# Performance work log

Measured on AMD Instinct MI355X. Metric: run time of the kernel, lower is better.

## Reference

```python
import jax, jax.numpy as jnp
import numpy as np

B, T, D, H = 2, 2048, 1024, 16
DH = D // H

def setup_inputs() -> dict:
    key = jax.random.key(0)
    ks = jax.random.split(key, 5)
    scale = 1.0 / np.sqrt(D)
    x = jax.random.normal(ks[0], (B, T, D), dtype=jnp.float32)
    Wq = jax.random.normal(ks[1], (D, D), dtype=jnp.float32) * scale
    Wk = jax.random.normal(ks[2], (D, D), dtype=jnp.float32) * scale
    Wv = jax.random.normal(ks[3], (D, D), dtype=jnp.float32) * scale
    Wo = jax.random.normal(ks[4], (D, D), dtype=jnp.float32) * scale
    # causal mask: True means masked (matches torch masked_fill semantics)
    mask = jnp.triu(jnp.ones((T, T), dtype=bool), k=1)
    return {"x": x, "mask": mask, "Wq": Wq, "Wk": Wk, "Wv": Wv, "Wo": Wo}

def reference(x, mask, Wq, Wk, Wv, Wo):
    b, t, c = x.shape
    # projections -> [B, H, T, DH]
    def split_heads(y):
        return y.reshape(b, t, H, DH).transpose(0, 2, 1, 3)
    q = split_heads(x @ Wq)
    k = split_heads(x @ Wk)
    v = split_heads(x @ Wv)
    # scores [B, H, T, T]
    att = jnp.einsum('bhqd,bhkd->bhqk', q, k) / jnp.sqrt(jnp.float32(DH))
    att = jnp.where(mask, -jnp.inf, att)
    att = jax.nn.softmax(att, axis=-1)
    # dropout=0.0 (eval-mode determinism)
    out = jnp.einsum('bhqk,bhkd->bhqd', att, v)
    out = out.transpose(0, 2, 1, 3).reshape(b, t, c)
    return out @ Wo
```

## Files before the change

kernel.cpp:

```cpp
#include <hip/hip_runtime.h>
#include <stdint.h>

typedef unsigned short u16;
typedef unsigned int u32;
typedef __attribute__((ext_vector_type(8))) short s16x8;
typedef __attribute__((ext_vector_type(4))) float f32x4;
typedef __attribute__((ext_vector_type(8))) unsigned short u16x8;
typedef __attribute__((ext_vector_type(4))) unsigned short u16x4;

#define T_ 2048
#define D_ 1024
#define H_ 16
#define DH_ 64

#define QSCALE_LOG2E 0.18033688011112042f

#if __has_builtin(__builtin_amdgcn_exp2f)
#define EXP2(x) __builtin_amdgcn_exp2f(x)
#else
#define EXP2(x) exp2f(x)
#endif

__device__ __forceinline__ float bf2f(u16 u) {
    union { unsigned int i; float f; } x; x.i = ((unsigned int)u) << 16; return x.f;
}
__device__ __forceinline__ u16 f2bf(float f) {
    union { float f; unsigned int i; } x; x.f = f;
    unsigned int u = x.i;
    u += 0x7fffu + ((u >> 16) & 1u);
    return (u16)(u >> 16);
}
__device__ __forceinline__ u32 pack_rn(float a, float b) {
    union { float f; u32 u; } ua, ub; ua.f = a; ub.f = b;
    return ((ua.u + 0x8000u) >> 16) | ((ub.u + 0x8000u) & 0xffff0000u);
}

__device__ __forceinline__ void gload16(const u16* g, u16* l) {
    __builtin_amdgcn_global_load_lds(
        (const __attribute__((address_space(1))) void*)g,
        (__attribute__((address_space(3))) void*)l,
        16, 0, 0);
}

__global__ __launch_bounds__(256) void cvt_x_kernel(const float* __restrict__ x,
                                                    u16* __restrict__ xb) {
    int i = (blockIdx.x * 256 + threadIdx.x) * 4;
    float4 v = *(const float4*)(x + i);
    u16x4 o;
    o[0] = f2bf(v.x); o[1] = f2bf(v.y); o[2] = f2bf(v.z); o[3] = f2bf(v.w);
    *(u16x4*)(xb + i) = o;
}

__global__ __launch_bounds__(256) void transpose_w_kernel(const float* __restrict__ Wq,
                                                          const float* __restrict__ Wk,
                                                          const float* __restrict__ Wv,
                                                          const float* __restrict__ Wo,
                                                          u16* __restrict__ WT) {
    __shared__ float tile[32][33];
    int s = blockIdx.z;
    const float* W = (s == 0) ? Wq : (s == 1) ? Wk : (s == 2) ? Wv : Wo;
    int n0 = blockIdx.x * 32;
    int k0 = blockIdx.y * 32;
    int tx = threadIdx.x, ty = threadIdx.y;
    #pragma unroll
    for (int j = 0; j < 32; j += 8)
        tile[ty + j][tx] = W[(k0 + ty + j) * D_ + n0 + tx];
    __syncthreads();
    u16* dst = WT + (size_t)s * D_ * D_;
    #pragma unroll
    for (int j = 0; j < 32; j += 8)
        dst[(n0 + ty + j) * D_ + k0 + tx] = f2bf(tile[tx][ty + j]);
}

__global__ __launch_bounds__(256) void gemm_qkv(const u16* __restrict__ A,
                                                const u16* __restrict__ Bt,
                                                u16* __restrict__ Qw,
                                                u16* __restrict__ Kw,
                                                u16* __restrict__ Vw) {
    __shared__ __align__(16) u16 As[2][128 * 32];
    __shared__ __align__(16) u16 Bs[2][128 * 32];
    const int m0 = blockIdx.x * 128, n0 = blockIdx.y * 128;
    int tid = threadIdx.x;
    int w = tid >> 6, lane = tid & 63, quad = lane >> 4, l15 = lane & 15;
    int wr = w >> 1, wc = w & 1;

    int nb0 = (w << 7), nb1 = nb0 + 64;
    int c0 = nb0 + lane, c1 = nb1 + lane;
    int r0 = c0 >> 2, k0off = (c0 & 3) << 3;
    int r1 = c1 >> 2, k1off = (c1 & 3) << 3;
    const u16* Ar0 = A + (size_t)(m0 + r0) * D_ + k0off;
    const u16* Ar1 = A + (size_t)(m0 + r1) * D_ + k1off;
    const u16* Br0 = Bt + (size_t)(n0 + r0) * D_ + k0off;
    const u16* Br1 = Bt + (size_t)(n0 + r1) * D_ + k1off;

    f32x4 acc[4][4];
    #pragma unroll
    for (int mi = 0; mi < 4; ++mi)
        #pragma unroll
        for (int ni = 0; ni < 4; ++ni) acc[mi][ni] = (f32x4){0.f, 0.f, 0.f, 0.f};

    gload16(Ar0, &As[0][nb0 << 3]);
    gload16(Ar1, &As[0][nb1 << 3]);
    gload16(Br0, &Bs[0][nb0 << 3]);
    gload16(Br1, &Bs[0][nb1 << 3]);

    for (int k0 = 0; k0 < D_; k0 += 32) {
        int buf = (k0 >> 5) & 1;
        __syncthreads();
        if (k0 + 32 < D_) {
            int kn = k0 + 32;
            gload16(Ar0 + kn, &As[buf ^ 1][nb0 << 3]);
            gload16(Ar1 + kn, &As[buf ^ 1][nb1 << 3]);
            gload16(Br0 + kn, &Bs[buf ^ 1][nb0 << 3]);
            gload16(Br1 + kn, &Bs[buf ^ 1][nb1 << 3]);
        }
        s16x8 af[4], bf[4];
        #pragma unroll
        for (int mi = 0; mi < 4; ++mi)
            af[mi] = *(const s16x8*)&As[buf][((wr * 64 + mi * 16 + l15) << 5) + (quad << 3)];
        #pragma unroll
        for (int ni = 0; ni < 4; ++ni)
            bf[ni] = *(const s16x8*)&Bs[buf][((wc * 64 + ni * 16 + l15) << 5) + (quad << 3)];
        #pragma unroll
        for (int mi = 0; mi < 4; ++mi)
            #pragma unroll
            for (int ni = 0; ni < 4; ++ni)
                acc[mi][ni] = __builtin_amdgcn_mfma_f32_16x16x32_bf16(af[mi], bf[ni],
                                                                      acc[mi][ni], 0, 0, 0);
    }

    #pragma unroll
    for (int mi = 0; mi < 4; ++mi) {
        int mbase = m0 + wr * 64 + mi * 16 + quad * 4;
        #pragma unroll
        for (int ni = 0; ni < 4; ++ni) {
            int n = n0 + wc * 64 + ni * 16 + l15;
            int b = mbase >> 11, t0 = mbase & 2047;
            int sel = n >> 10, nn = n & 1023;
            int h = nn >> 6, dh = nn & 63;
            int bhidx = (b << 4) + h;
            if (sel == 0) {
                #pragma unroll
                for (int r = 0; r < 4; ++r)
                    Qw[(size_t)(bhidx * T_ + t0 + r) * DH_ + dh] =
                        f2bf(acc[mi][ni][r] * QSCALE_LOG2E);
            } else if (sel == 1) {
                #pragma unroll
                for (int r = 0; r < 4; ++r)
                    Kw[(size_t)(bhidx * T_ + t0 + r) * DH_ + dh] = f2bf(acc[mi][ni][r]);
            } else {
                uint2 pk;
                pk.x = pack_rn(acc[mi][ni][0], acc[mi][ni][1]);
                pk.y = pack_rn(acc[mi][ni][2], acc[mi][ni][3]);
                *(uint2*)(Vw + ((size_t)bhidx * DH_ + dh) * T_ + t0) = pk;
            }
        }
    }
}

__global__ __launch_bounds__(256) void gemm_out(const u16* __restrict__ A,
                                                const u16* __restrict__ Bt,
                                                float* __restrict__ Cout) {
    __shared__ __align__(16) u16 As[2][128 * 32];
    __shared__ __align__(16) u16 Bs[2][64 * 32];
    const int m0 = blockIdx.x * 128, n0 = blockIdx.y * 64;
    int tid = threadIdx.x;
    int w = tid >> 6, lane = tid & 63, quad = lane >> 4, l15 = lane & 15;

    int nbA0 = (w << 7), nbA1 = nbA0 + 64, nbB = (w << 6);
    int cA0 = nbA0 + lane, cA1 = nbA1 + lane, cB = nbB + lane;
    const u16* ArA0 = A + (size_t)(m0 + (cA0 >> 2)) * D_ + ((cA0 & 3) << 3);
    const u16* ArA1 = A + (size_t)(m0 + (cA1 >> 2)) * D_ + ((cA1 & 3) << 3);
    const u16* BrB  = Bt + (size_t)(n0 + (cB >> 2)) * D_ + ((cB & 3) << 3);

    f32x4 acc[2][4];
    #pragma unroll
    for (int mi = 0; mi < 2; ++mi)
        #pragma unroll
        for (int ni = 0; ni < 4; ++ni) acc[mi][ni] = (f32x4){0.f, 0.f, 0.f, 0.f};

    gload16(ArA0, &As[0][nbA0 << 3]);
    gload16(ArA1, &As[0][nbA1 << 3]);
    gload16(BrB,  &Bs[0][nbB << 3]);

    for (int k0 = 0; k0 < D_; k0 += 32) {
        int buf = (k0 >> 5) & 1;
        __syncthreads();
        if (k0 + 32 < D_) {
            int kn = k0 + 32;
            gload16(ArA0 + kn, &As[buf ^ 1][nbA0 << 3]);
            gload16(ArA1 + kn, &As[buf ^ 1][nbA1 << 3]);
            gload16(BrB + kn,  &Bs[buf ^ 1][nbB << 3]);
        }
        s16x8 af[2], bf[4];
        #pragma unroll
        for (int mi = 0; mi < 2; ++mi)
            af[mi] = *(const s16x8*)&As[buf][((w * 32 + mi * 16 + l15) << 5) + (quad << 3)];
        #pragma unroll
        for (int ni = 0; ni < 4; ++ni)
            bf[ni] = *(const s16x8*)&Bs[buf][((ni * 16 + l15) << 5) + (quad << 3)];
        #pragma unroll
        for (int mi = 0; mi < 2; ++mi)
            #pragma unroll
            for (int ni = 0; ni < 4; ++ni)
                acc[mi][ni] = __builtin_amdgcn_mfma_f32_16x16x32_bf16(af[mi], bf[ni],
                                                                      acc[mi][ni], 0, 0, 0);
    }

    #pragma unroll
    for (int mi = 0; mi < 2; ++mi) {
        int mbase = m0 + w * 32 + mi * 16 + quad * 4;
        #pragma unroll
        for (int ni = 0; ni < 4; ++ni) {
            int n = n0 + ni * 16 + l15;
            #pragma unroll
            for (int r = 0; r < 4; ++r)
                Cout[(size_t)(mbase + r) * D_ + n] = acc[mi][ni][r];
        }
    }
}

__global__ __launch_bounds__(256) void attn_mfma_kernel(const u16* __restrict__ Qg,
                                                        const u16* __restrict__ Kg,
                                                        const u16* __restrict__ Vt,
                                                        u16* __restrict__ Opart,
                                                        float* __restrict__ lpart) {
    __shared__ __align__(16) u16 Kbuf[2][64 * 64];
    __shared__ __align__(16) u16 Vbuf[2][64 * 64];
    __shared__ __align__(16) u16 Ps[4][2][16][72];

    int blk = blockIdx.x;
    int xcd = blk & 7, slot = blk >> 3;
    int bh = (xcd << 2) + (slot / 40);
    int x  = slot % 40;
    int BX, c;
    if (x < 4)       { BX = x;                    c = 0; }
    else if (x < 12) { BX = 4 + ((x - 4) >> 1);   c = (x - 4) & 1; }
    else if (x < 24) { BX = 8 + (x - 12) / 3;     c = (x - 12) % 3; }
    else             { BX = 12 + ((x - 24) >> 2); c = (x - 24) & 3; }
    int kstart = c << 3;
    int ktm = 2 * BX + 1;
    int kend = min(kstart + 8, ktm + 1);

    int tid = threadIdx.x;
    int w = tid >> 6, lane = tid & 63, quad = lane >> 4, l15 = lane & 15;
    int q0 = BX << 7;
    int qA = q0 + 16 * w;
    int qB = q0 + 64 + 16 * w;

    const u16* Qb = Qg + (size_t)bh * T_ * DH_;
    const u16* Kb = Kg + (size_t)bh * T_ * DH_;
    const u16* Vb = Vt + (size_t)bh * DH_ * T_;

    s16x8 qa0 = *(const s16x8*)(Qb + (size_t)(qA + l15) * DH_ + quad * 8);
    s16x8 qa1 = *(const s16x8*)(Qb + (size_t)(qA + l15) * DH_ + quad * 8 + 32);
    s16x8 qc0 = *(const s16x8*)(Qb + (size_t)(qB + l15) * DH_ + quad * 8);
    s16x8 qc1 = *(const s16x8*)(Qb + (size_t)(qB + l15) * DH_ + quad * 8 + 32);

    int nb0 = (w << 7), nb1 = nb0 + 64;
    int n0c = nb0 + lane, n1c = nb1 + lane;
    int r0 = n0c >> 3, c0s = n0c & 7, g0 = (r0 << 3) + (c0s ^ (r0 & 7));
    int r1 = n1c >> 3, c1s = n1c & 7, g1 = (r1 << 3) + (c1s ^ (r1 & 7));

    {
        int kb0 = kstart << 6;
        const u16* Ktile = Kb + (size_t)kb0 * DH_;
        gload16(Ktile + (g0 << 3), &Kbuf[0][nb0 << 3]);
        gload16(Ktile + (g1 << 3), &Kbuf[0][nb1 << 3]);
        gload16(Vb + (size_t)r0 * T_ + kb0 + ((g0 & 7) << 3), &Vbuf[0][nb0 << 3]);
        gload16(Vb + (size_t)r1 * T_ + kb0 + ((g1 & 7) << 3), &Vbuf[0][nb1 << 3]);
    }

    f32x4 oA[4] = {{0.f,0.f,0.f,0.f},{0.f,0.f,0.f,0.f},{0.f,0.f,0.f,0.f},{0.f,0.f,0.f,0.f}};
    f32x4 oB[4] = {{0.f,0.f,0.f,0.f},{0.f,0.f,0.f,0.f},{0.f,0.f,0.f,0.f},{0.f,0.f,0.f,0.f}};
    float lA = 0.f, lB = 0.f;

    for (int kt = kstart; kt < kend; ++kt) {
        int buf = (kt - kstart) & 1;
        __syncthreads();

        if (kt + 1 < kend) {
            int kb2 = (kt + 1) << 6;
            const u16* Ktile = Kb + (size_t)kb2 * DH_;
            gload16(Ktile + (g0 << 3), &Kbuf[buf ^ 1][nb0 << 3]);
            gload16(Ktile + (g1 << 3), &Kbuf[buf ^ 1][nb1 << 3]);
            gload16(Vb + (size_t)r0 * T_ + kb2 + ((g0 & 7) << 3), &Vbuf[buf ^ 1][nb0 << 3]);
            gload16(Vb + (size_t)r1 * T_ + kb2 + ((g1 & 7) << 3), &Vbuf[buf ^ 1][nb1 << 3]);
        }

        f32x4 sA[4], sB[4];
        #pragma unroll
        for (int g = 0; g < 4; ++g) {
            int r = (g << 4) + l15;
            int cc = quad ^ (r & 7);
            s16x8 ka0 = *(const s16x8*)&Kbuf[buf][((r << 3) + cc) << 3];
            s16x8 ka1 = *(const s16x8*)&Kbuf[buf][((r << 3) + (cc ^ 4)) << 3];
            f32x4 z = {0.f, 0.f, 0.f, 0.f};
            sA[g] = __builtin_amdgcn_mfma_f32_16x16x32_bf16(ka0, qa0, z, 0, 0, 0);
            sA[g] = __builtin_amdgcn_mfma_f32_16x16x32_bf16(ka1, qa1, sA[g], 0, 0, 0);
            sB[g] = __builtin_amdgcn_mfma_f32_16x16x32_bf16(ka0, qc0, z, 0, 0, 0);
            sB[g] = __builtin_amdgcn_mfma_f32_16x16x32_bf16(ka1, qc1, sB[g], 0, 0, 0);
        }

        if (kt >= ktm - 1) {
            int rA = q0 + 16 * w + l15 - (kt << 6);
            #pragma unroll
            for (int g = 0; g < 4; ++g)
                #pragma unroll
                for (int r = 0; r < 4; ++r)
                    if ((g << 4) + (quad << 2) + r > rA) sA[g][r] = -INFINITY;
        }
        if (kt == ktm) {
            int rB = 16 * w + l15;
            #pragma unroll
            for (int g = 0; g < 4; ++g)
                #pragma unroll
                for (int r = 0; r < 4; ++r)
                    if ((g << 4) + (quad << 2) + r > rB) sB[g][r] = -INFINITY;
        }

        #pragma unroll
        for (int g = 0; g < 4; ++g)
            #pragma unroll
            for (int r = 0; r < 4; ++r) {
                float pA = EXP2(sA[g][r]); sA[g][r] = pA; lA += pA;
                float pB = EXP2(sB[g][r]); sB[g][r] = pB; lB += pB;
            }

        #pragma unroll
        for (int g = 0; g < 4; ++g) {
            uint2 pkA, pkB;
            pkA.x = pack_rn(sA[g][0], sA[g][1]); pkA.y = pack_rn(sA[g][2], sA[g][3]);
            pkB.x = pack_rn(sB[g][0], sB[g][1]); pkB.y = pack_rn(sB[g][2], sB[g][3]);
            *(uint2*)&Ps[w][0][l15][g * 16 + quad * 4] = pkA;
            *(uint2*)&Ps[w][1][l15][g * 16 + quad * 4] = pkB;
        }
        s16x8 pa0 = *(const s16x8*)&Ps[w][0][l15][quad * 8];
        s16x8 pa1 = *(const s16x8*)&Ps[w][0][l15][quad * 8 + 32];
        s16x8 pc0 = *(const s16x8*)&Ps[w][1][l15][quad * 8];
        s16x8 pc1 = *(const s16x8*)&Ps[w][1][l15][quad * 8 + 32];

        #pragma unroll
        for (int g = 0; g < 4; ++g) {
            int r = (g << 4) + l15;
            int cc = quad ^ (r & 7);
            s16x8 va0 = *(const s16x8*)&Vbuf[buf][((r << 3) + cc) << 3];
            s16x8 va1 = *(const s16x8*)&Vbuf[buf][((r << 3) + (cc ^ 4)) << 3];
            oA[g] = __builtin_amdgcn_mfma_f32_16x16x32_bf16(va0, pa0, oA[g], 0, 0, 0);
            oA[g] = __builtin_amdgcn_mfma_f32_16x16x32_bf16(va1, pa1, oA[g], 0, 0, 0);
            oB[g] = __builtin_amdgcn_mfma_f32_16x16x32_bf16(va0, pc0, oB[g], 0, 0, 0);
            oB[g] = __builtin_amdgcn_mfma_f32_16x16x32_bf16(va1, pc1, oB[g], 0, 0, 0);
        }
    }

    lA += __shfl_xor(lA, 16); lA += __shfl_xor(lA, 32);
    lB += __shfl_xor(lB, 16); lB += __shfl_xor(lB, 32);
    int slotid = ((bh << 4) + BX) * 4 + c;
    u16* dA = Opart + ((size_t)slotid * 128 + 16 * w + l15) * 64;
    u16* dB = dA + 64 * 64;
    #pragma unroll
    for (int g = 0; g < 4; ++g) {
        uint2 pk;
        pk.x = pack_rn(oA[g][0], oA[g][1]); pk.y = pack_rn(oA[g][2], oA[g][3]);
        *(uint2*)(dA + (g << 4) + (quad << 2)) = pk;
        pk.x = pack_rn(oB[g][0], oB[g][1]); pk.y = pack_rn(oB[g][2], oB[g][3]);
        *(uint2*)(dB + (g << 4) + (quad << 2)) = pk;
    }
    if (quad == 0) {
        lpart[(size_t)slotid * 128 + 16 * w + l15] = lA;
        lpart[(size_t)slotid * 128 + 64 + 16 * w + l15] = lB;
    }
}

__global__ __launch_bounds__(256) void reduce_attn(const u16* __restrict__ Opart,
                                                   const float* __restrict__ lpart,
                                                   u16* __restrict__ att) {
    int BX = blockIdx.x, bh = blockIdx.y;
    int nch = (BX >> 2) + 1;
    int tid = threadIdx.x;
    int row = tid >> 1, dh0 = (tid & 1) << 5;
    int slotbase = ((bh << 4) + BX) << 2;

    float acc[32];
    #pragma unroll
    for (int i = 0; i < 32; ++i) acc[i] = 0.f;
    float l = 0.f;
    for (int cc = 0; cc < nch; ++cc) {
        const u16* op = Opart + ((size_t)(slotbase + cc) * 128 + row) * 64 + dh0;
        #pragma unroll
        for (int v = 0; v < 4; ++v) {
            u16x8 o8 = *(const u16x8*)(op + v * 8);
            #pragma unroll
            for (int j = 0; j < 8; ++j) acc[v * 8 + j] += bf2f(o8[j]);
        }
        l += lpart[(size_t)(slotbase + cc) * 128 + row];
    }
    float inv = 1.f / l;
    int b = bh >> 4, h = bh & 15;
    int q = (BX << 7) + row;
    u16* dst = att + ((size_t)(b * T_) + q) * D_ + (h << 6) + dh0;
    #pragma unroll
    for (int v = 0; v < 2; ++v) {
        u16x8 o8;
        #pragma unroll
        for (int j = 0; j < 8; ++j) o8[j] = f2bf(acc[v * 16 + j * 2] * inv),
                                    o8[j] = o8[j];
        #pragma unroll
        for (int j = 0; j < 8; ++j) o8[j] = f2bf(acc[v * 16 + j] * inv);
        u16x8 o8b;
        #pragma unroll
        for (int j = 0; j < 8; ++j) o8b[j] = f2bf(acc[v * 16 + 8 + j] * inv);
        *(u16x8*)(dst + v * 16) = o8;
        *(u16x8*)(dst + v * 16 + 8) = o8b;
    }
}

extern "C" void kernel_launch(void* const* d_in, const int* in_sizes, int n_in,
                              void* d_out, int out_size, void* d_ws, size_t ws_size,
                              hipStream_t stream) {
    const float* x  = (const float*)d_in[0];
    const float* Wq = (const float*)d_in[2];
    const float* Wk = (const float*)d_in[3];
    const float* Wv = (const float*)d_in[4];
    const float* Wo = (const float*)d_in[5];
    float* out = (float*)d_out;

    char* ws = (char*)d_ws;
    u16*   xb    = (u16*)(ws);
    u16*   WT    = (u16*)(ws + (8ull  << 20));
    u16*   Qw    = (u16*)(ws + (16ull << 20));
    u16*   Kw    = (u16*)(ws + (24ull << 20));
    u16*   Vw    = (u16*)(ws + (32ull << 20));
    u16*   att   = (u16*)(ws + (40ull << 20));
    u16*   Opart = (u16*)(ws + (48ull << 20));
    float* lpart = (float*)(ws + (82ull << 20));

    cvt_x_kernel<<<dim3(4096), dim3(256), 0, stream>>>(x, xb);
    transpose_w_kernel<<<dim3(32, 32, 4), dim3(32, 8), 0, stream>>>(Wq, Wk, Wv, Wo, WT);
    gemm_qkv<<<dim3(32, 24), dim3(256), 0, stream>>>(xb, WT, Qw, Kw, Vw);
    attn_mfma_kernel<<<dim3(1280), dim3(256), 0, stream>>>(Qw, Kw, Vw, Opart, lpart);
    reduce_attn<<<dim3(16, 32), dim3(256), 0, stream>>>(Opart, lpart, att);
    gemm_out<<<dim3(32, 16), dim3(256), 0, stream>>>(att, WT + 3ull * 1048576ull, out);
}
```

Measured before the change: 200.0 us.

## Swizzle GEMM LDS tiles and merge input preparation kernels

Applies an XOR swizzle to the k-chunk placement in the LDS tiles of both projection GEMMs, so that fragment reads no longer hit the same banks. The swizzle is applied on the global source offset, so the direct-to-LDS loads stay linear. The x conversion and the weight transpose are merged into one launch, and the reduce store loop is simplified. This adds index arithmetic per load.

Measured after the change: 195.2 us. -2.4%, faster.

```diff
diff --git a/kernel.cpp b/kernel.cpp
--- a/kernel.cpp
+++ b/kernel.cpp
@@ -42,34 +42,37 @@
         16, 0, 0);
 }
 
-__global__ __launch_bounds__(256) void cvt_x_kernel(const float* __restrict__ x,
-                                                    u16* __restrict__ xb) {
-    int i = (blockIdx.x * 256 + threadIdx.x) * 4;
-    float4 v = *(const float4*)(x + i);
-    u16x4 o;
-    o[0] = f2bf(v.x); o[1] = f2bf(v.y); o[2] = f2bf(v.z); o[3] = f2bf(v.w);
-    *(u16x4*)(xb + i) = o;
-}
-
-__global__ __launch_bounds__(256) void transpose_w_kernel(const float* __restrict__ Wq,
-                                                          const float* __restrict__ Wk,
-                                                          const float* __restrict__ Wv,
-                                                          const float* __restrict__ Wo,
-                                                          u16* __restrict__ WT) {
+__global__ __launch_bounds__(256) void prep_kernel(const float* __restrict__ x,
+                                                   const float* __restrict__ Wq,
+                                                   const float* __restrict__ Wk,
+                                                   const float* __restrict__ Wv,
+                                                   const float* __restrict__ Wo,
+                                                   u16* __restrict__ xb,
+                                                   u16* __restrict__ WT) {
     __shared__ float tile[32][33];
-    int s = blockIdx.z;
-    const float* W = (s == 0) ? Wq : (s == 1) ? Wk : (s == 2) ? Wv : Wo;
-    int n0 = blockIdx.x * 32;
-    int k0 = blockIdx.y * 32;
-    int tx = threadIdx.x, ty = threadIdx.y;
-    #pragma unroll
-    for (int j = 0; j < 32; j += 8)
-        tile[ty + j][tx] = W[(k0 + ty + j) * D_ + n0 + tx];
-    __syncthreads();
-    u16* dst = WT + (size_t)s * D_ * D_;
-    #pragma unroll
-    for (int j = 0; j < 32; j += 8)
-        dst[(n0 + ty + j) * D_ + k0 + tx] = f2bf(tile[tx][ty + j]);
+    int blk = blockIdx.x;
+    if (blk < 4096) {
+        int i = (blk * 256 + threadIdx.x) * 4;
+        float4 v = *(const float4*)(x + i);
+        u16x4 o;
+        o[0] = f2bf(v.x); o[1] = f2bf(v.y); o[2] = f2bf(v.z); o[3] = f2bf(v.w);
+        *(u16x4*)(xb + i) = o;
+    } else {
+        int t = blk - 4096;
+        int s = t >> 10;
+        const float* W = (s == 0) ? Wq : (s == 1) ? Wk : (s == 2) ? Wv : Wo;
+        int n0 = ((t >> 5) & 31) * 32;
+        int k0 = (t & 31) * 32;
+        int tx = threadIdx.x & 31, ty = threadIdx.x >> 5;
+        #pragma unroll
+        for (int j = 0; j < 32; j += 8)
+            tile[ty + j][tx] = W[(k0 + ty + j) * D_ + n0 + tx];
+        __syncthreads();
+        u16* dst = WT + (size_t)s * D_ * D_;
+        #pragma unroll
+        for (int j = 0; j < 32; j += 8)
+            dst[(n0 + ty + j) * D_ + k0 + tx] = f2bf(tile[tx][ty + j]);
+    }
 }
 
 __global__ __launch_bounds__(256) void gemm_qkv(const u16* __restrict__ A,
@@ -86,8 +89,8 @@
 
     int nb0 = (w << 7), nb1 = nb0 + 64;
     int c0 = nb0 + lane, c1 = nb1 + lane;
-    int r0 = c0 >> 2, k0off = (c0 & 3) << 3;
-    int r1 = c1 >> 2, k1off = (c1 & 3) << 3;
+    int r0 = c0 >> 2, k0off = (((c0 & 3) ^ ((r0 >> 1) & 3)) << 3);
+    int r1 = c1 >> 2, k1off = (((c1 & 3) ^ ((r1 >> 1) & 3)) << 3);
     const u16* Ar0 = A + (size_t)(m0 + r0) * D_ + k0off;
     const u16* Ar1 = A + (size_t)(m0 + r1) * D_ + k1off;
     const u16* Br0 = Bt + (size_t)(n0 + r0) * D_ + k0off;
@@ -116,11 +119,15 @@
         }
         s16x8 af[4], bf[4];
         #pragma unroll
-        for (int mi = 0; mi < 4; ++mi)
-            af[mi] = *(const s16x8*)&As[buf][((wr * 64 + mi * 16 + l15) << 5) + (quad << 3)];
-        #pragma unroll
-        for (int ni = 0; ni < 4; ++ni)
-            bf[ni] = *(const s16x8*)&Bs[buf][((wc * 64 + ni * 16 + l15) << 5) + (quad << 3)];
+        for (int mi = 0; mi < 4; ++mi) {
+            int R = wr * 64 + mi * 16 + l15;
+            af[mi] = *(const s16x8*)&As[buf][((R << 2) | (quad ^ ((R >> 1) & 3))) << 3];
+        }
+        #pragma unroll
+        for (int ni = 0; ni < 4; ++ni) {
+            int R = wc * 64 + ni * 16 + l15;
+            bf[ni] = *(const s16x8*)&Bs[buf][((R << 2) | (quad ^ ((R >> 1) & 3))) << 3];
+        }
         #pragma unroll
         for (int mi = 0; mi < 4; ++mi)
             #pragma unroll
@@ -169,9 +176,12 @@
 
     int nbA0 = (w << 7), nbA1 = nbA0 + 64, nbB = (w << 6);
     int cA0 = nbA0 + lane, cA1 = nbA1 + lane, cB = nbB + lane;
-    const u16* ArA0 = A + (size_t)(m0 + (cA0 >> 2)) * D_ + ((cA0 & 3) << 3);
-    const u16* ArA1 = A + (size_t)(m0 + (cA1 >> 2)) * D_ + ((cA1 & 3) << 3);
-    const u16* BrB  = Bt + (size_t)(n0 + (cB >> 2)) * D_ + ((cB & 3) << 3);
+    int rA0 = cA0 >> 2, kA0 = (((cA0 & 3) ^ ((rA0 >> 1) & 3)) << 3);
+    int rA1 = cA1 >> 2, kA1 = (((cA1 & 3) ^ ((rA1 >> 1) & 3)) << 3);
+    int rB  = cB >> 2,  kB  = (((cB  & 3) ^ ((rB  >> 1) & 3)) << 3);
+    const u16* ArA0 = A + (size_t)(m0 + rA0) * D_ + kA0;
+    const u16* ArA1 = A + (size_t)(m0 + rA1) * D_ + kA1;
+    const u16* BrB  = Bt + (size_t)(n0 + rB) * D_ + kB;
 
     f32x4 acc[2][4];
     #pragma unroll
@@ -194,11 +204,15 @@
         }
         s16x8 af[2], bf[4];
         #pragma unroll
-        for (int mi = 0; mi < 2; ++mi)
-            af[mi] = *(const s16x8*)&As[buf][((w * 32 + mi * 16 + l15) << 5) + (quad << 3)];
-        #pragma unroll
-        for (int ni = 0; ni < 4; ++ni)
-            bf[ni] = *(const s16x8*)&Bs[buf][((ni * 16 + l15) << 5) + (quad << 3)];
+        for (int mi = 0; mi < 2; ++mi) {
+            int R = w * 32 + mi * 16 + l15;
+            af[mi] = *(const s16x8*)&As[buf][((R << 2) | (quad ^ ((R >> 1) & 3))) << 3];
+        }
+        #pragma unroll
+        for (int ni = 0; ni < 4; ++ni) {
+            int R = ni * 16 + l15;
+            bf[ni] = *(const s16x8*)&Bs[buf][((R << 2) | (quad ^ ((R >> 1) & 3))) << 3];
+        }
         #pragma unroll
         for (int mi = 0; mi < 2; ++mi)
             #pragma unroll
@@ -400,18 +414,11 @@
     int q = (BX << 7) + row;
     u16* dst = att + ((size_t)(b * T_) + q) * D_ + (h << 6) + dh0;
     #pragma unroll
-    for (int v = 0; v < 2; ++v) {
+    for (int v = 0; v < 4; ++v) {
         u16x8 o8;
         #pragma unroll
-        for (int j = 0; j < 8; ++j) o8[j] = f2bf(acc[v * 16 + j * 2] * inv),
-                                    o8[j] = o8[j];
-        #pragma unroll
-        for (int j = 0; j < 8; ++j) o8[j] = f2bf(acc[v * 16 + j] * inv);
-        u16x8 o8b;
-        #pragma unroll
-        for (int j = 0; j < 8; ++j) o8b[j] = f2bf(acc[v * 16 + 8 + j] * inv);
-        *(u16x8*)(dst + v * 16) = o8;
-        *(u16x8*)(dst + v * 16 + 8) = o8b;
+        for (int j = 0; j < 8; ++j) o8[j] = f2bf(acc[v * 8 + j] * inv);
+        *(u16x8*)(dst + v * 8) = o8;
     }
 }
 
@@ -435,8 +442,7 @@
     u16*   Opart = (u16*)(ws + (48ull << 20));
     float* lpart = (float*)(ws + (82ull << 20));
 
-    cvt_x_kernel<<<dim3(4096), dim3(256), 0, stream>>>(x, xb);
-    transpose_w_kernel<<<dim3(32, 32, 4), dim3(32, 8), 0, stream>>>(Wq, Wk, Wv, Wo, WT);
+    prep_kernel<<<dim3(8192), dim3(256), 0, stream>>>(x, Wq, Wk, Wv, Wo, xb, WT);
     gemm_qkv<<<dim3(32, 24), dim3(256), 0, stream>>>(xb, WT, Qw, Kw, Vw);
     attn_mfma_kernel<<<dim3(1280), dim3(256), 0, stream>>>(Qw, Kw, Vw, Opart, lpart);
     reduce_attn<<<dim3(16, 32), dim3(256), 0, stream>>>(Opart, lpart, att);
```
